# Kernel tuning notes

Hardware: AMD Instinct MI355X
Metric: run time of the kernel (lower is better)

Reference implementation:

```python
import jax, jax.numpy as jnp
import numpy as np

N, S, D, H, NF, E = 65536, 24, 64, 4, 256, 1048576
Hd = D // H
EPS = 1e-5


def _pe_table(nf, d):
    pe = np.zeros((nf, d), np.float32)
    pos = np.arange(nf, dtype=np.float32)[:, None]
    div = np.exp(np.arange(0, d, 2, dtype=np.float32) * -(np.log(10000.0) / d))
    pe[:, 0::2] = np.sin(pos * div)
    pe[:, 1::2] = np.cos(pos * div)
    return jnp.asarray(pe)


def setup_inputs() -> dict:
    key = jax.random.key(0)
    ks = iter(jax.random.split(key, 64))
    g = lambda shape: jax.random.normal(next(ks), shape, jnp.float32) * 0.02
    z = lambda shape: jnp.zeros(shape, jnp.float32)
    o = lambda shape: jnp.ones(shape, jnp.float32)
    inp = {
        'x': jax.random.normal(next(ks), (N, S), jnp.float32),
        'edge_index': jax.random.randint(next(ks), (2, E), 0, N, jnp.int32),
        'Wi': g((S, D)), 'bi': z((D,)), 'pe': _pe_table(NF, D),
        # per-head TransformerConv params (H separate convs, heads=1 each)
        'Wq': g((H, D, Hd)), 'Wk': g((H, D, Hd)), 'Wv': g((H, D, Hd)),
        'bq': z((H, Hd)), 'bk': z((H, Hd)), 'bv': z((H, Hd)),
        'Ws': g((H, D, Hd)), 'bs': z((H, Hd)),
        'Wo': g((D, D)), 'bo': z((D,)), 'gln_g': o((D,)), 'gln_b': z((D,)),
        # temporal MHA + FFN
        'Wqt': g((D, D)), 'Wkt': g((D, D)), 'Wvt': g((D, D)),
        'bqt': z((D,)), 'bkt': z((D,)), 'bvt': z((D,)),
        'Wot': g((D, D)), 'bot': z((D,)),
        'ln1_g': o((D,)), 'ln1_b': z((D,)),
        'W1': g((D, 2 * D)), 'b1': z((2 * D,)), 'W2': g((2 * D, D)), 'b2': z((D,)),
        'ln2_g': o((D,)), 'ln2_b': z((D,)),
        # aggregation + prediction head
        'Wa1': g((NF * D, D)), 'ba1': z((D,)), 'Wa2': g((D, D // 2)), 'ba2': z((D // 2,)),
        'Wh1': g((D // 2, D // 4)), 'bh1': z((D // 4,)), 'Wh2': g((D // 4, 1)), 'bh2': z((1,)),
    }
    return inp


def _ln(x, g, b):
    m = jnp.mean(x, axis=-1, keepdims=True)
    v = jnp.var(x, axis=-1, keepdims=True)
    return (x - m) * jax.lax.rsqrt(v + EPS) * g + b


def reference(x, edge_index, Wi, bi, pe, Wq, Wk, Wv, bq, bk, bv, Ws, bs, Wo, bo,
              gln_g, gln_b, Wqt, Wkt, Wvt, bqt, bkt, bvt, Wot, bot, ln1_g, ln1_b,
              W1, b1, W2, b2, ln2_g, ln2_b, Wa1, ba1, Wa2, ba2, Wh1, bh1, Wh2, bh2):
    n, nf, d = x.shape[0], pe.shape[0], pe.shape[1]
    bsz = n // nf
    scale = 1.0 / np.sqrt(Hd).astype(np.float32)

    # input projection + positional encoding (repeated per graph)
    h = x @ Wi + bi + jnp.tile(pe, (bsz, 1))  # [N, D]

    # ---- multi-head TransformerConv graph attention (gather-softmax-scatter) ----
    src, dst = edge_index[0], edge_index[1]
    q = jnp.einsum('nd,hdk->nhk', h, Wq) + bq  # [N,H,Hd]
    k = jnp.einsum('nd,hdk->nhk', h, Wk) + bk
    v = jnp.einsum('nd,hdk->nhk', h, Wv) + bv
    logits = jnp.sum(q[dst] * k[src], axis=-1) * scale  # [E,H]
    m = jax.ops.segment_max(logits, dst, num_segments=N)  # [N,H]
    ex = jnp.exp(logits - m[dst])
    denom = jax.ops.segment_sum(ex, dst, num_segments=N)  # [N,H]
    alpha = ex / denom[dst]
    agg = jax.ops.segment_sum(alpha[:, :, None] * v[src], dst, num_segments=N)  # [N,H,Hd]
    skip = jnp.einsum('nd,hdk->nhk', h, Ws) + bs  # root weight (lin_skip)
    out = (agg + skip).reshape(n, d) @ Wo + bo
    h = _ln(out + h, gln_g, gln_b)  # residual (in_dim == out_dim)

    # ---- temporal transformer over the NF node axis ----
    xt = h.reshape(bsz, nf, d)
    qt = (xt @ Wqt + bqt).reshape(bsz, nf, H, Hd)
    kt = (xt @ Wkt + bkt).reshape(bsz, nf, H, Hd)
    vt = (xt @ Wvt + bvt).reshape(bsz, nf, H, Hd)
    sc = jnp.einsum('bihd,bjhd->bhij', qt, kt) * scale
    a = jax.nn.softmax(sc, axis=-1)
    attn = jnp.einsum('bhij,bjhd->bihd', a, vt).reshape(bsz, nf, d)
    attn = attn @ Wot + bot
    xt = _ln(xt + attn, ln1_g, ln1_b)
    ff = jax.nn.relu(xt @ W1 + b1) @ W2 + b2
    xt = _ln(xt + ff, ln2_g, ln2_b)

    # ---- aggregation + prediction head ----
    xf = xt.reshape(bsz, nf * d)
    a1 = jax.nn.relu(xf @ Wa1 + ba1)
    a2 = jax.nn.relu(a1 @ Wa2 + ba2)
    h1 = jax.nn.relu(a2 @ Wh1 + bh1)
    out = jax.nn.sigmoid(h1 @ Wh2 + bh2)
    return out.squeeze(-1)  # [B]
```

## Files before the change

### kernel.cpp

```cpp
#include <hip/hip_runtime.h>
#include <hip/hip_fp16.h>
#include <math.h>

#define NN 65536
#define SIN 24
#define DD 64
#define HH 4
#define HDIM 16
#define NFRM 256
#define NE 1048576
#define BSZ 256
#define EPSLN 1e-5f
#define SCL 0.25f
#define AKS 32

typedef __attribute__((ext_vector_type(8))) short bf16x8;
typedef __attribute__((ext_vector_type(4))) float f32x4;

__device__ __forceinline__ unsigned short f2bf(float f) {
  unsigned u = __float_as_uint(f);
  return (unsigned short)((u + 0x7FFFu + ((u >> 16) & 1u)) >> 16);
}
__device__ __forceinline__ float bf2f(unsigned short b) {
  return __uint_as_float(((unsigned)b) << 16);
}
__device__ __forceinline__ float bflo(unsigned u) {
  return __uint_as_float(u << 16);
}
__device__ __forceinline__ float bfhi(unsigned u) {
  return __uint_as_float(u & 0xFFFF0000u);
}
__device__ __forceinline__ unsigned f2e5(float f) {
  unsigned short h = __half_as_ushort(__float2half(f));
  unsigned r = (unsigned)h + 0x7Fu + ((h >> 8) & 1u);
  return (r >> 8) & 0xFFu;
}
__device__ __forceinline__ float h2fb(unsigned short b) {
  return __half2float(__ushort_as_half(b));
}
#define KLO(u) h2fb((unsigned short)((u) & 0xFF00u))
#define KHI(u) h2fb((unsigned short)(((u) >> 16) & 0xFF00u))
#define VLO(u) h2fb((unsigned short)(((u) << 8) & 0xFF00u))
#define VHI(u) h2fb((unsigned short)(((u) >> 8) & 0xFF00u))

__device__ __forceinline__ void stage_bf(const unsigned short* __restrict__ src,
                                         unsigned short* dst, int n8, int DK, int ST, int tid) {
  int dk8 = DK >> 3;
  for (int idx = tid; idx < n8; idx += 256) {
    int row = idx / dk8, c = (idx % dk8) * 8;
    *(uint4*)(dst + row * ST + c) = *(const uint4*)(src + (size_t)row * DK + c);
  }
}

__global__ void k_wprep(const float* __restrict__ Wo, const float* __restrict__ Wot,
                        const float* __restrict__ Wqt, const float* __restrict__ Wkt,
                        const float* __restrict__ Wvt, const float* __restrict__ W1,
                        const float* __restrict__ W2, const float* __restrict__ Wq,
                        const float* __restrict__ Wk, const float* __restrict__ Wv,
                        const float* __restrict__ Wsk, unsigned short* __restrict__ wt) {
  int i = blockIdx.x * 256 + threadIdx.x;
  if (i >= 53248) return;
  float v;
  if (i < 4096)       { int t = i;         int j = t >> 6, d = t & 63; v = Wo[d * 64 + j]; }
  else if (i < 8192)  { int t = i - 4096;  int j = t >> 6, d = t & 63; v = Wot[d * 64 + j]; }
  else if (i < 12288) { int t = i - 8192;  int j = t >> 6, d = t & 63; v = Wqt[d * 64 + j]; }
  else if (i < 16384) { int t = i - 12288; int j = t >> 6, d = t & 63; v = Wkt[d * 64 + j]; }
  else if (i < 20480) { int t = i - 16384; int j = t >> 6, d = t & 63; v = Wvt[d * 64 + j]; }
  else if (i < 28672) { int t = i - 20480; int j = t >> 6, d = t & 63; v = W1[d * 128 + j]; }
  else if (i < 36864) { int t = i - 28672; int j = t >> 7, d = t & 127; v = W2[d * 64 + j]; }
  else if (i < 40960) { int t = i - 36864; int j = t >> 6, d = t & 63; v = Wq[(j >> 4) * 1024 + d * 16 + (j & 15)]; }
  else if (i < 45056) { int t = i - 40960; int j = t >> 6, d = t & 63; v = Wk[(j >> 4) * 1024 + d * 16 + (j & 15)]; }
  else if (i < 49152) { int t = i - 45056; int j = t >> 6, d = t & 63; v = Wv[(j >> 4) * 1024 + d * 16 + (j & 15)]; }
  else                { int t = i - 49152; int j = t >> 6, d = t & 63; v = Wsk[(j >> 4) * 1024 + d * 16 + (j & 15)]; }
  wt[i] = f2bf(v);
}

__global__ void k_wprep2(const float* __restrict__ Wa1, unsigned short* __restrict__ wa1t) {
  __shared__ float tile[64][65];
  int kb = blockIdx.x;
  int t = threadIdx.x;
  int c = t & 63, r0 = t >> 6;
  int k0 = kb * 64;
#pragma unroll
  for (int i = 0; i < 16; ++i) {
    int r = r0 + i * 4;
    tile[r][c] = Wa1[(size_t)(k0 + r) * 64 + c];
  }
  __syncthreads();
#pragma unroll
  for (int i = 0; i < 16; ++i) {
    int o = r0 + i * 4;
    wa1t[(size_t)o * 16384 + k0 + c] = f2bf(tile[c][o]);
  }
}

__global__ void __launch_bounds__(256)
k_qkvs_m(const float* __restrict__ x, const float* __restrict__ Wi,
         const float* __restrict__ bi, const float* __restrict__ pe,
         const unsigned short* __restrict__ wt,
         const float* __restrict__ bq, const float* __restrict__ bk,
         const float* __restrict__ bv, const float* __restrict__ bs,
         float* __restrict__ f_h, unsigned short* __restrict__ us_q,
         unsigned short* __restrict__ kv8, unsigned short* __restrict__ us_sk) {
  __shared__ unsigned short Xs[64 * 72];
  __shared__ unsigned short Ws4[4 * 64 * 72];
  float* Xs32 = (float*)Ws4;
  int tid = threadIdx.x;
  int n0 = blockIdx.x * 64;
  for (int idx = tid; idx < 64 * SIN; idx += 256) {
    int row = idx / SIN, c = idx % SIN;
    Xs32[row * 25 + c] = x[(size_t)(n0 + row) * SIN + c];
  }
  __syncthreads();
  int j = tid & 63, r0 = tid >> 6;
  float hacc[16];
  {
    float bb = bi[j];
#pragma unroll
    for (int i = 0; i < 16; ++i) {
      int row = r0 + 4 * i;
      hacc[i] = bb + pe[((n0 + row) & (NFRM - 1)) * DD + j];
    }
    for (int s = 0; s < SIN; ++s) {
      float w = Wi[s * DD + j];
#pragma unroll
      for (int i = 0; i < 16; ++i)
        hacc[i] += Xs32[(r0 + 4 * i) * 25 + s] * w;
    }
  }
  __syncthreads();
#pragma unroll
  for (int i = 0; i < 16; ++i) {
    int row = r0 + 4 * i;
    f_h[(size_t)(n0 + row) * DD + j] = hacc[i];
    Xs[row * 72 + j] = f2bf(hacc[i]);
  }
  stage_bf(wt + 36864, Ws4, 64 * 8, 64, 72, tid);
  stage_bf(wt + 40960, Ws4 + 4608, 64 * 8, 64, 72, tid);
  stage_bf(wt + 45056, Ws4 + 9216, 64 * 8, 64, 72, tid);
  stage_bf(wt + 49152, Ws4 + 13824, 64 * 8, 64, 72, tid);
  __syncthreads();
  int lane = tid & 63, w = tid >> 6;
  int c = lane & 15, g = lane >> 4;
  f32x4 aq[4], ak[4], av[4], as_[4];
#pragma unroll
  for (int jj = 0; jj < 4; ++jj) {
#pragma unroll
    for (int r = 0; r < 4; ++r) { aq[jj][r] = 0.f; ak[jj][r] = 0.f; av[jj][r] = 0.f; as_[jj][r] = 0.f; }
  }
  const unsigned short* xrow = Xs + (w * 16 + c) * 72 + g * 8;
#pragma unroll
  for (int kk = 0; kk < 2; ++kk) {
    bf16x8 af = *(const bf16x8*)(xrow + kk * 32);
#pragma unroll
    for (int jj = 0; jj < 4; ++jj) {
      int boff = (jj * 16 + c) * 72 + kk * 32 + g * 8;
      aq[jj] = __builtin_amdgcn_mfma_f32_16x16x32_bf16(af, *(const bf16x8*)(Ws4 + boff), aq[jj], 0, 0, 0);
      ak[jj] = __builtin_amdgcn_mfma_f32_16x16x32_bf16(af, *(const bf16x8*)(Ws4 + 4608 + boff), ak[jj], 0, 0, 0);
      av[jj] = __builtin_amdgcn_mfma_f32_16x16x32_bf16(af, *(const bf16x8*)(Ws4 + 9216 + boff), av[jj], 0, 0, 0);
      as_[jj] = __builtin_amdgcn_mfma_f32_16x16x32_bf16(af, *(const bf16x8*)(Ws4 + 13824 + boff), as_[jj], 0, 0, 0);
    }
  }
  int rowb = n0 + w * 16 + 4 * g;
#pragma unroll
  for (int jj = 0; jj < 4; ++jj) {
    int col = jj * 16 + c;
    float bqj = bq[col], bkj = bk[col], bvj = bv[col], bsj = bs[col];
#pragma unroll
    for (int r = 0; r < 4; ++r) {
      size_t o = (size_t)(rowb + r) * 64 + col;
      us_q[o] = f2bf(aq[jj][r] + bqj);
      kv8[o] = (unsigned short)((f2e5(ak[jj][r] + bkj) << 8) | f2e5(av[jj][r] + bvj));
      us_sk[o] = f2bf(as_[jj][r] + bsj);
    }
  }
}

__global__ void k_hist(const int* __restrict__ ei, int* __restrict__ hist) {
  __shared__ int h[256];
  int t = threadIdx.x;
  h[t] = 0;
  __syncthreads();
  int base = blockIdx.x * 4096;
#pragma unroll
  for (int r = 0; r < 16; ++r)
    atomicAdd(&h[ei[NE + base + r * 256 + t] >> 8], 1);
  __syncthreads();
  hist[t * 256 + blockIdx.x] = h[t];
}

__global__ void k_hscan(int* __restrict__ hist, int* __restrict__ btot) {
  __shared__ int s[256];
  int t = threadIdx.x, bkt = blockIdx.x;
  int v = hist[bkt * 256 + t];
  s[t] = v; __syncthreads();
  for (int off = 1; off < 256; off <<= 1) {
    int x = (t >= off) ? s[t - off] : 0;
    __syncthreads();
    s[t] += x;
    __syncthreads();
  }
  hist[bkt * 256 + t] = s[t] - v;
  if (t == 255) btot[bkt] = s[255];
}

__global__ void k_bscan(const int* __restrict__ btot, int* __restrict__ bbase) {
  __shared__ int s[256];
  int t = threadIdx.x;
  int v = btot[t];
  s[t] = v; __syncthreads();
  for (int off = 1; off < 256; off <<= 1) {
    int x = (t >= off) ? s[t - off] : 0;
    __syncthreads();
    s[t] += x;
    __syncthreads();
  }
  bbase[t] = s[t] - v;
}

__global__ void k_passB(const int* __restrict__ ei, const int* __restrict__ hist,
                        const int* __restrict__ bbase, int* __restrict__ pairs) {
  __shared__ int cur[256];
  int t = threadIdx.x;
  cur[t] = bbase[t] + hist[t * 256 + blockIdx.x];
  __syncthreads();
  int base = blockIdx.x * 4096;
#pragma unroll
  for (int r = 0; r < 16; ++r) {
    int e = base + r * 256 + t;
    int src = ei[e], dst = ei[NE + e];
    int pos = atomicAdd(&cur[dst >> 8], 1);
    pairs[pos] = ((dst & 255) << 16) | src;
  }
}

__global__ void k_passC(const int* __restrict__ pairs, const int* __restrict__ bbase,
                        const int* __restrict__ btot, int* __restrict__ rowptr,
                        int* __restrict__ srcs) {
  __shared__ int cnt[256];
  __shared__ int s[256];
  int t = threadIdx.x, bkt = blockIdx.x;
  cnt[t] = 0;
  __syncthreads();
  int base = bbase[bkt], n = btot[bkt];
  for (int i = t; i < n; i += 256) atomicAdd(&cnt[pairs[base + i] >> 16], 1);
  __syncthreads();
  int v = cnt[t];
  s[t] = v; __syncthreads();
  for (int off = 1; off < 256; off <<= 1) {
    int x = (t >= off) ? s[t - off] : 0;
    __syncthreads();
    s[t] += x;
    __syncthreads();
  }
  int rp = base + s[t] - v;
  rowptr[bkt * 256 + t] = rp;
  if (bkt == 0 && t == 0) rowptr[NN] = NE;
  __syncthreads();
  cnt[t] = rp;
  __syncthreads();
  for (int i = t; i < n; i += 256) {
    int p = pairs[base + i];
    int pos = atomicAdd(&cnt[p >> 16], 1);
    srcs[pos] = p & 0xFFFF;
  }
}

__global__ void __launch_bounds__(256)
k_gattn(const unsigned short* __restrict__ us_q, const unsigned short* __restrict__ kv8,
        const int* __restrict__ rowptr, const int* __restrict__ srcs,
        const unsigned short* __restrict__ us_sk, unsigned short* __restrict__ tmpb) {
  __shared__ float red[8][32][17];
  int tid = threadIdx.x;
  int lane = tid & 63;
  int slot = (tid >> 5) & 7;
  int e = (lane >> 2) & 7, h = lane & 3;
  int dst = (blockIdx.x << 3) + slot;
  float qv[16];
  {
    const uint4* qp = (const uint4*)(us_q + (size_t)dst * 64 + h * 16);
    uint4 q0 = qp[0], q1 = qp[1];
    qv[0] = bflo(q0.x); qv[1] = bfhi(q0.x); qv[2] = bflo(q0.y); qv[3] = bfhi(q0.y);
    qv[4] = bflo(q0.z); qv[5] = bfhi(q0.z); qv[6] = bflo(q0.w); qv[7] = bfhi(q0.w);
    qv[8] = bflo(q1.x); qv[9] = bfhi(q1.x); qv[10] = bflo(q1.y); qv[11] = bfhi(q1.y);
    qv[12] = bflo(q1.z); qv[13] = bfhi(q1.z); qv[14] = bflo(q1.w); qv[15] = bfhi(q1.w);
  }
  int beg = rowptr[dst], end = rowptr[dst + 1];
  float l = 0.f;
  float acc[16];
#pragma unroll
  for (int i = 0; i < 16; ++i) acc[i] = 0.f;

  int idx = beg + e;
  int src = (idx < end) ? srcs[idx] : 0;
  const uint4* kp = (const uint4*)(kv8 + (size_t)src * 64 + h * 16);
  uint4 A = kp[0], Bv = kp[1];
  for (;;) {
    int nidx = idx + 8;
    bool any_next = __any(nidx < end);
    uint4 nA, nB;
    if (any_next) {
      int nsrc = (nidx < end) ? srcs[nidx] : 0;
      const uint4* np = (const uint4*)(kv8 + (size_t)nsrc * 64 + h * 16);
      nA = np[0]; nB = np[1];
    }
    bool valid = idx < end;
    float s;
    s  = KLO(A.x) * qv[0]   + KHI(A.x) * qv[1]   + KLO(A.y) * qv[2]   + KHI(A.y) * qv[3];
    s += KLO(A.z) * qv[4]   + KHI(A.z) * qv[5]   + KLO(A.w) * qv[6]   + KHI(A.w) * qv[7];
    s += KLO(Bv.x) * qv[8]  + KHI(Bv.x) * qv[9]  + KLO(Bv.y) * qv[10] + KHI(Bv.y) * qv[11];
    s += KLO(Bv.z) * qv[12] + KHI(Bv.z) * qv[13] + KLO(Bv.w) * qv[14] + KHI(Bv.w) * qv[15];
    float pex = valid ? __expf(s * SCL) : 0.f;
    l += pex;
    acc[0]  += pex * VLO(A.x);  acc[1]  += pex * VHI(A.x);
    acc[2]  += pex * VLO(A.y);  acc[3]  += pex * VHI(A.y);
    acc[4]  += pex * VLO(A.z);  acc[5]  += pex * VHI(A.z);
    acc[6]  += pex * VLO(A.w);  acc[7]  += pex * VHI(A.w);
    acc[8]  += pex * VLO(Bv.x); acc[9]  += pex * VHI(Bv.x);
    acc[10] += pex * VLO(Bv.y); acc[11] += pex * VHI(Bv.y);
    acc[12] += pex * VLO(Bv.z); acc[13] += pex * VHI(Bv.z);
    acc[14] += pex * VLO(Bv.w); acc[15] += pex * VHI(Bv.w);
    if (!any_next) break;
    A = nA; Bv = nB;
    idx = nidx;
  }
  l += __shfl_xor(l, 4); l += __shfl_xor(l, 8); l += __shfl_xor(l, 16);
  float* rw = &red[slot][lane & 31][0];
#pragma unroll
  for (int i = 0; i < 16; ++i) rw[i] = acc[i];
  int r32 = lane & 31;
  int h0 = r32 >> 4, i0 = r32 & 15;
  float l0 = __shfl(l, (lane & 32) + h0);
  float l1 = __shfl(l, (lane & 32) + h0 + 2);
  float s0 = 0.f, s1 = 0.f;
#pragma unroll
  for (int ep = 0; ep < 8; ++ep) {
    s0 += red[slot][ep * 4 + h0][i0];
    s1 += red[slot][ep * 4 + h0 + 2][i0];
  }
  bool nonempty = end > beg;
  float a0 = nonempty ? s0 / l0 : 0.f;
  float a1 = nonempty ? s1 / l1 : 0.f;
  size_t o0 = (size_t)dst * 64 + r32;
  tmpb[o0] = f2bf(a0 + bf2f(us_sk[o0]));
  tmpb[o0 + 32] = f2bf(a1 + bf2f(us_sk[o0 + 32]));
}

__global__ void __launch_bounds__(256)
k_mlqkvt(const unsigned short* __restrict__ in1, const unsigned short* __restrict__ wt,
         const float* __restrict__ bias, const float* __restrict__ gam,
         const float* __restrict__ bet, float* __restrict__ io,
         const float* __restrict__ bqt, const float* __restrict__ bkt,
         const float* __restrict__ bvt,
         unsigned short* __restrict__ qt, unsigned short* __restrict__ kt,
         unsigned short* __restrict__ vt) {
  __shared__ unsigned short A[64 * 72];
  __shared__ unsigned short B[3 * 64 * 72];
  int tid = threadIdx.x;
  int n0 = blockIdx.x * 64;
  stage_bf(in1 + (size_t)n0 * 64, A, 64 * 8, 64, 72, tid);
  stage_bf(wt + 0, B, 64 * 8, 64, 72, tid);
  __syncthreads();
  int lane = tid & 63, w = tid >> 6;
  int c = lane & 15, g = lane >> 4;
  f32x4 acc[4];
#pragma unroll
  for (int j = 0; j < 4; ++j) { acc[j][0] = 0.f; acc[j][1] = 0.f; acc[j][2] = 0.f; acc[j][3] = 0.f; }
  const unsigned short* xrow = A + (w * 16 + c) * 72 + g * 8;
#pragma unroll
  for (int kk = 0; kk < 2; ++kk) {
    bf16x8 af = *(const bf16x8*)(xrow + kk * 32);
#pragma unroll
    for (int j = 0; j < 4; ++j)
      acc[j] = __builtin_amdgcn_mfma_f32_16x16x32_bf16(af,
                 *(const bf16x8*)(B + (j * 16 + c) * 72 + kk * 32 + g * 8), acc[j], 0, 0, 0);
  }
  int rowb = n0 + w * 16 + 4 * g;
  float o[4][4];
#pragma unroll
  for (int j = 0; j < 4; ++j) {
    int col = j * 16 + c;
    float bb = bias[col];
#pragma unroll
    for (int r = 0; r < 4; ++r)
      o[j][r] = acc[j][r] + bb + io[(size_t)(rowb + r) * 64 + col];
  }
#pragma unroll
  for (int r = 0; r < 4; ++r) {
    float s = (o[0][r] + o[1][r]) + (o[2][r] + o[3][r]);
    float s2 = (o[0][r] * o[0][r] + o[1][r] * o[1][r]) + (o[2][r] * o[2][r] + o[3][r] * o[3][r]);
#pragma unroll
    for (int off = 1; off <= 8; off <<= 1) {
      s += __shfl_xor(s, off);
      s2 += __shfl_xor(s2, off);
    }
    float mean = s * (1.0f / 64.0f);
    float var = s2 * (1.0f / 64.0f) - mean * mean;
    float rs = rsqrtf(var + EPSLN);
#pragma unroll
    for (int j = 0; j < 4; ++j)
      o[j][r] = (o[j][r] - mean) * rs * gam[j * 16 + c] + bet[j * 16 + c];
  }
  __syncthreads();
#pragma unroll
  for (int j = 0; j < 4; ++j) {
    int col = j * 16 + c;
#pragma unroll
    for (int r = 0; r < 4; ++r) {
      io[(size_t)(rowb + r) * 64 + col] = o[j][r];
      A[(w * 16 + 4 * g + r) * 72 + col] = f2bf(o[j][r]);
    }
  }
  stage_bf(wt + 8192, B, 64 * 8, 64, 72, tid);
  stage_bf(wt + 12288, B + 4608, 64 * 8, 64, 72, tid);
  stage_bf(wt + 16384, B + 9216, 64 * 8, 64, 72, tid);
  __syncthreads();
  f32x4 aq[4], ak[4], av[4];
#pragma unroll
  for (int j = 0; j < 4; ++j) {
#pragma unroll
    for (int r = 0; r < 4; ++r) { aq[j][r] = 0.f; ak[j][r] = 0.f; av[j][r] = 0.f; }
  }
#pragma unroll
  for (int kk = 0; kk < 2; ++kk) {
    bf16x8 af = *(const bf16x8*)(xrow + kk * 32);
#pragma unroll
    for (int j = 0; j < 4; ++j) {
      int boff = (j * 16 + c) * 72 + kk * 32 + g * 8;
      aq[j] = __builtin_amdgcn_mfma_f32_16x16x32_bf16(af, *(const bf16x8*)(B + boff), aq[j], 0, 0, 0);
      ak[j] = __builtin_amdgcn_mfma_f32_16x16x32_bf16(af, *(const bf16x8*)(B + 4608 + boff), ak[j], 0, 0, 0);
      av[j] = __builtin_amdgcn_mfma_f32_16x16x32_bf16(af, *(const bf16x8*)(B + 9216 + boff), av[j], 0, 0, 0);
    }
  }
#pragma unroll
  for (int j = 0; j < 4; ++j) {
    int col = j * 16 + c;
    float bqj = bqt[col], bkj = bkt[col], bvj = bvt[col];
#pragma unroll
    for (int r = 0; r < 4; ++r) {
      size_t oo = (size_t)(rowb + r) * 64 + col;
      qt[oo] = f2bf(aq[j][r] + bqj);
      kt[oo] = f2bf(ak[j][r] + bkj);
      vt[oo] = f2bf(av[j][r] + bvj);
    }
  }
}

#define VST 20
#define PST 40
__global__ void __launch_bounds__(256)
k_tattn(const unsigned short* __restrict__ qtb, const unsigned short* __restrict__ ktb,
        const unsigned short* __restrict__ vtb, unsigned short* __restrict__ attnb) {
  int b = blockIdx.x >> 2, hh = blockIdx.x & 3;
  __shared__ unsigned short Qs[NFRM][16];
  __shared__ unsigned short Ks[NFRM][16];
  __shared__ unsigned short Vs[NFRM][VST];
  __shared__ unsigned short Ps[4][16][PST];
  int t = threadIdx.x;
  int wv = t >> 6, lane = t & 63;
  int g = lane >> 4, c = lane & 15;
  {
    size_t src = ((size_t)b * NFRM + t) * DD + hh * 16;
    const uint4* qsrc = (const uint4*)(qtb + src);
    const uint4* ksrc = (const uint4*)(ktb + src);
    const uint2* vsrc = (const uint2*)(vtb + src);
    ((uint4*)Qs[t])[0] = qsrc[0]; ((uint4*)Qs[t])[1] = qsrc[1];
    ((uint4*)Ks[t])[0] = ksrc[0]; ((uint4*)Ks[t])[1] = ksrc[1];
    uint2* vdst = (uint2*)Vs[t];
    vdst[0] = vsrc[0]; vdst[1] = vsrc[1]; vdst[2] = vsrc[2]; vdst[3] = vsrc[3];
  }
  __syncthreads();
  const bf16x8 zf = {0, 0, 0, 0, 0, 0, 0, 0};
  unsigned short (*P)[PST] = Ps[wv];
  for (int qt0 = wv; qt0 < 16; qt0 += 4) {
    bf16x8 qf = zf;
    if (g < 2) qf = *(const bf16x8*)&Qs[qt0 * 16 + c][g * 8];
    f32x4 O = {0.f, 0.f, 0.f, 0.f};
    float lacc[4] = {0.f, 0.f, 0.f, 0.f};
    for (int jp = 0; jp < 8; ++jp) {
#pragma unroll
      for (int half = 0; half < 2; ++half) {
        int jt = jp * 2 + half;
        bf16x8 kf = zf;
        if (g < 2) kf = *(const bf16x8*)&Ks[jt * 16 + c][g * 8];
        f32x4 S = __builtin_amdgcn_mfma_f32_16x16x32_bf16(qf, kf,
                    (f32x4){0.f, 0.f, 0.f, 0.f}, 0, 0, 0);
#pragma unroll
        for (int r = 0; r < 4; ++r) {
          float p = __expf(S[r] * SCL);
          lacc[r] += p;
          P[4 * g + r][half * 16 + c] = f2bf(p);
        }
      }
      bf16x8 pf = *(const bf16x8*)&P[c][g * 8];
      bf16x8 vf;
#pragma unroll
      for (int i = 0; i < 8; ++i) vf[i] = (short)Vs[jp * 32 + g * 8 + i][c];
      O = __builtin_amdgcn_mfma_f32_16x16x32_bf16(pf, vf, O, 0, 0, 0);
    }
#pragma unroll
    for (int r = 0; r < 4; ++r) {
      float s = lacc[r];
      s += __shfl_xor(s, 1); s += __shfl_xor(s, 2);
      s += __shfl_xor(s, 4); s += __shfl_xor(s, 8);
      lacc[r] = 1.0f / s;
    }
    size_t obase = ((size_t)b * NFRM + qt0 * 16) * DD + hh * 16;
#pragma unroll
    for (int r = 0; r < 4; ++r)
      attnb[obase + (size_t)(4 * g + r) * DD + c] = f2bf(O[r] * lacc[r]);
  }
}

__global__ void __launch_bounds__(256)
k_blk2(const unsigned short* __restrict__ attn, const unsigned short* __restrict__ wt,
       const float* __restrict__ res, const float* __restrict__ bot,
       const float* __restrict__ l1g, const float* __restrict__ l1b,
       const float* __restrict__ b1, const float* __restrict__ b2,
       const float* __restrict__ l2g, const float* __restrict__ l2b,
       unsigned short* __restrict__ xtb) {
  __shared__ unsigned short XLs[64 * 72];
  __shared__ unsigned short BufW[128 * 72];
  __shared__ unsigned short BufX[64 * 136];
  int tid = threadIdx.x;
  int n0 = blockIdx.x * 64;
  int lane = tid & 63, w = tid >> 6;
  int c = lane & 15, g = lane >> 4;
  int rowb = n0 + w * 16 + 4 * g;
  stage_bf(attn + (size_t)n0 * 64, BufX, 64 * 8, 64, 72, tid);
  stage_bf(wt + 4096, BufW, 64 * 8, 64, 72, tid);
  __syncthreads();
  f32x4 acc[4];
#pragma unroll
  for (int j = 0; j < 4; ++j) { acc[j][0] = 0.f; acc[j][1] = 0.f; acc[j][2] = 0.f; acc[j][3] = 0.f; }
  const unsigned short* xrow = BufX + (w * 16 + c) * 72 + g * 8;
#pragma unroll
  for (int kk = 0; kk < 2; ++kk) {
    bf16x8 af = *(const bf16x8*)(xrow + kk * 32);
#pragma unroll
    for (int j = 0; j < 4; ++j)
      acc[j] = __builtin_amdgcn_mfma_f32_16x16x32_bf16(af,
                 *(const bf16x8*)(BufW + (j * 16 + c) * 72 + kk * 32 + g * 8), acc[j], 0, 0, 0);
  }
  float x[4][4];
#pragma unroll
  for (int j = 0; j < 4; ++j) {
    int col = j * 16 + c;
    float bb = bot[col];
#pragma unroll
    for (int r = 0; r < 4; ++r)
      x[j][r] = acc[j][r] + bb + res[(size_t)(rowb + r) * 64 + col];
  }
#pragma unroll
  for (int r = 0; r < 4; ++r) {
    float s = (x[0][r] + x[1][r]) + (x[2][r] + x[3][r]);
    float s2 = (x[0][r] * x[0][r] + x[1][r] * x[1][r]) + (x[2][r] * x[2][r] + x[3][r] * x[3][r]);
#pragma unroll
    for (int off = 1; off <= 8; off <<= 1) {
      s += __shfl_xor(s, off);
      s2 += __shfl_xor(s2, off);
    }
    float mean = s * (1.0f / 64.0f);
    float var = s2 * (1.0f / 64.0f) - mean * mean;
    float rs = rsqrtf(var + EPSLN);
#pragma unroll
    for (int j = 0; j < 4; ++j)
      x[j][r] = (x[j][r] - mean) * rs * l1g[j * 16 + c] + l1b[j * 16 + c];
  }
  __syncthreads();
#pragma unroll
  for (int j = 0; j < 4; ++j)
#pragma unroll
    for (int r = 0; r < 4; ++r)
      XLs[(w * 16 + 4 * g + r) * 72 + j * 16 + c] = f2bf(x[j][r]);
  stage_bf(wt + 20480, BufW, 128 * 8, 64, 72, tid);
  __syncthreads();
  f32x4 ua[8];
#pragma unroll
  for (int j = 0; j < 8; ++j) { ua[j][0] = 0.f; ua[j][1] = 0.f; ua[j][2] = 0.f; ua[j][3] = 0.f; }
  const unsigned short* xrow2 = XLs + (w * 16 + c) * 72 + g * 8;
#pragma unroll
  for (int kk = 0; kk < 2; ++kk) {
    bf16x8 af = *(const bf16x8*)(xrow2 + kk * 32);
#pragma unroll
    for (int j = 0; j < 8; ++j)
      ua[j] = __builtin_amdgcn_mfma_f32_16x16x32_bf16(af,
                *(const bf16x8*)(BufW + (j * 16 + c) * 72 + kk * 32 + g * 8), ua[j], 0, 0, 0);
  }
#pragma unroll
  for (int j = 0; j < 8; ++j) {
    int col = j * 16 + c;
    float bb = b1[col];
#pragma unroll
    for (int r = 0; r < 4; ++r)
      BufX[(w * 16 + 4 * g + r) * 136 + col] = f2bf(fmaxf(ua[j][r] + bb, 0.f));
  }
  __syncthreads();
  stage_bf(wt + 28672, BufW, 64 * 16, 128, 136, tid);
  __syncthreads();
  f32x4 ya[4];
#pragma unroll
  for (int j = 0; j < 4; ++j) { ya[j][0] = 0.f; ya[j][1] = 0.f; ya[j][2] = 0.f; ya[j][3] = 0.f; }
  const unsigned short* urow = BufX + (w * 16 + c) * 136 + g * 8;
#pragma unroll
  for (int kk = 0; kk < 4; ++kk) {
    bf16x8 af = *(const bf16x8*)(urow + kk * 32);
#pragma unroll
    for (int j = 0; j < 4; ++j)
      ya[j] = __builtin_amdgcn_mfma_f32_16x16x32_bf16(af,
                *(const bf16x8*)(BufW + (j * 16 + c) * 136 + kk * 32 + g * 8), ya[j], 0, 0, 0);
  }
  float o2[4][4];
#pragma unroll
  for (int j = 0; j < 4; ++j) {
    int col = j * 16 + c;
    float bb = b2[col];
#pragma unroll
    for (int r = 0; r < 4; ++r)
      o2[j][r] = ya[j][r] + bb + x[j][r];
  }
#pragma unroll
  for (int r = 0; r < 4; ++r) {
    float s = (o2[0][r] + o2[1][r]) + (o2[2][r] + o2[3][r]);
    float s2 = (o2[0][r] * o2[0][r] + o2[1][r] * o2[1][r]) + (o2[2][r] * o2[2][r] + o2[3][r] * o2[3][r]);
#pragma unroll
    for (int off = 1; off <= 8; off <<= 1) {
      s += __shfl_xor(s, off);
      s2 += __shfl_xor(s2, off);
    }
    float mean = s * (1.0f / 64.0f);
    float var = s2 * (1.0f / 64.0f) - mean * mean;
    float rs = rsqrtf(var + EPSLN);
#pragma unroll
    for (int j = 0; j < 4; ++j)
      xtb[(size_t)(rowb + r) * 64 + j * 16 + c] =
          f2bf((o2[j][r] - mean) * rs * l2g[j * 16 + c] + l2b[j * 16 + c]);
  }
}

__global__ void __launch_bounds__(256)
k_agg1a_m(const unsigned short* __restrict__ xtb, const unsigned short* __restrict__ wa1t,
          float* __restrict__ part) {
  int ks = blockIdx.x >> 2, mt = blockIdx.x & 3;
  int t = threadIdx.x, lane = t & 63, w = t >> 6;
  int c = lane & 15, g = lane >> 4;
  int m0 = mt * 64;
  int k0 = ks * 512;
  f32x4 acc[4];
#pragma unroll
  for (int j = 0; j < 4; ++j) { acc[j][0] = 0.f; acc[j][1] = 0.f; acc[j][2] = 0.f; acc[j][3] = 0.f; }
  const unsigned short* arow = xtb + (size_t)(m0 + w * 16 + c) * 16384 + k0 + g * 8;
  const unsigned short* brow = wa1t + (size_t)c * 16384 + k0 + g * 8;
#pragma unroll 4
  for (int kk = 0; kk < 16; ++kk) {
    bf16x8 af = *(const bf16x8*)(arow + kk * 32);
#pragma unroll
    for (int j = 0; j < 4; ++j)
      acc[j] = __builtin_amdgcn_mfma_f32_16x16x32_bf16(af,
                 *(const bf16x8*)(brow + (size_t)j * 16 * 16384 + kk * 32), acc[j], 0, 0, 0);
  }
  int rowb = m0 + w * 16 + 4 * g;
#pragma unroll
  for (int j = 0; j < 4; ++j)
#pragma unroll
    for (int r = 0; r < 4; ++r)
      part[(size_t)ks * (BSZ * DD) + (size_t)(rowb + r) * 64 + j * 16 + c] = acc[j][r];
}

__global__ void k_head(const float* __restrict__ part, const float* __restrict__ ba1,
                       const float* __restrict__ Wa2, const float* __restrict__ ba2,
                       const float* __restrict__ Wh1, const float* __restrict__ bh1,
                       const float* __restrict__ Wh2, const float* __restrict__ bh2,
                       float* __restrict__ out) {
  int b = blockIdx.x, t = threadIdx.x;
  __shared__ float s1[64], s2[32], s3[16];
  float a0 = ba1[t];
#pragma unroll 8
  for (int ks = 0; ks < AKS; ++ks) a0 += part[(size_t)ks * (BSZ * DD) + b * 64 + t];
  s1[t] = fmaxf(a0, 0.f);
  __syncthreads();
  if (t < 32) {
    float a = ba2[t];
#pragma unroll 8
    for (int j = 0; j < 64; ++j) a += s1[j] * Wa2[j * 32 + t];
    s2[t] = fmaxf(a, 0.f);
  }
  __syncthreads();
  if (t < 16) {
    float a = bh1[t];
#pragma unroll
    for (int j = 0; j < 32; ++j) a += s2[j] * Wh1[j * 16 + t];
    s3[t] = fmaxf(a, 0.f);
  }
  __syncthreads();
  if (t == 0) {
    float a = bh2[0];
#pragma unroll
    for (int j = 0; j < 16; ++j) a += s3[j] * Wh2[j];
    out[b] = 1.0f / (1.0f + expf(-a));
  }
}

extern "C" void kernel_launch(void* const* d_in, const int* in_sizes, int n_in,
                              void* d_out, int out_size, void* d_ws, size_t ws_size,
                              hipStream_t stream) {
  const float* x   = (const float*)d_in[0];
  const int*   ei  = (const int*)d_in[1];
  const float* Wi  = (const float*)d_in[2];
  const float* bi  = (const float*)d_in[3];
  const float* pe  = (const float*)d_in[4];
  const float* Wq  = (const float*)d_in[5];
  const float* Wk  = (const float*)d_in[6];
  const float* Wv  = (const float*)d_in[7];
  const float* bq  = (const float*)d_in[8];
  const float* bk  = (const float*)d_in[9];
  const float* bv  = (const float*)d_in[10];
  const float* Ws  = (const float*)d_in[11];
  const float* bs  = (const float*)d_in[12];
  const float* Wo  = (const float*)d_in[13];
  const float* bo  = (const float*)d_in[14];
  const float* gg  = (const float*)d_in[15];
  const float* gb  = (const float*)d_in[16];
  const float* Wqt = (const float*)d_in[17];
  const float* Wkt = (const float*)d_in[18];
  const float* Wvt = (const float*)d_in[19];
  const float* bqt = (const float*)d_in[20];
  const float* bkt = (const float*)d_in[21];
  const float* bvt = (const float*)d_in[22];
  const float* Wot = (const float*)d_in[23];
  const float* bot = (const float*)d_in[24];
  const float* l1g = (const float*)d_in[25];
  const float* l1b = (const float*)d_in[26];
  const float* W1  = (const float*)d_in[27];
  const float* b1  = (const float*)d_in[28];
  const float* W2  = (const float*)d_in[29];
  const float* b2  = (const float*)d_in[30];
  const float* l2g = (const float*)d_in[31];
  const float* l2b = (const float*)d_in[32];
  const float* Wa1 = (const float*)d_in[33];
  const float* ba1 = (const float*)d_in[34];
  const float* Wa2 = (const float*)d_in[35];
  const float* ba2 = (const float*)d_in[36];
  const float* Wh1 = (const float*)d_in[37];
  const float* bh1 = (const float*)d_in[38];
  const float* Wh2 = (const float*)d_in[39];
  const float* bh2 = (const float*)d_in[40];
  float* out = (float*)d_out;

  const size_t ND = (size_t)NN * DD;

  float* wsf = (float*)d_ws;
  float* f_h = wsf;
  unsigned short* us_q  = (unsigned short*)(f_h + ND);
  unsigned short* kv8   = us_q + ND;
  unsigned short* us_sk = kv8 + ND;
  unsigned short* tmpb  = us_sk + ND;
  unsigned short* us_qt = tmpb + ND;
  unsigned short* us_kt = us_qt + ND;
  unsigned short* us_vt = us_kt + ND;
  unsigned short* attnb = us_vt + ND;
  unsigned short* xtb   = attnb + ND;
  float* f_part = (float*)(xtb + ND);
  int* i_srcs   = (int*)(f_part + (size_t)AKS * BSZ * DD);
  int* i_rowptr = i_srcs + NE;
  int* i_hist   = i_rowptr + NN + 1;
  int* i_btot   = i_hist + 65536;
  int* i_bbase  = i_btot + 256;
  int* i_pairs  = i_bbase + 256;
  unsigned short* wt = (unsigned short*)(i_pairs + NE);
  unsigned short* wa1t = wt + 53248;

  dim3 B(256);
  k_wprep<<<dim3(208), B, 0, stream>>>(Wo, Wot, Wqt, Wkt, Wvt, W1, W2, Wq, Wk, Wv, Ws, wt);
  k_wprep2<<<dim3(256), B, 0, stream>>>(Wa1, wa1t);
  k_qkvs_m<<<dim3(NN / 64), B, 0, stream>>>(x, Wi, bi, pe, wt, bq, bk, bv, bs,
                                            f_h, us_q, kv8, us_sk);
  k_hist <<<dim3(256), B, 0, stream>>>(ei, i_hist);
  k_hscan<<<dim3(256), B, 0, stream>>>(i_hist, i_btot);
  k_bscan<<<dim3(1),   B, 0, stream>>>(i_btot, i_bbase);
  k_passB<<<dim3(256), B, 0, stream>>>(ei, i_hist, i_bbase, i_pairs);
  k_passC<<<dim3(256), B, 0, stream>>>(i_pairs, i_bbase, i_btot, i_rowptr, i_srcs);
  k_gattn<<<dim3(NN / 8), B, 0, stream>>>(us_q, kv8, i_rowptr, i_srcs, us_sk, tmpb);
  k_mlqkvt<<<dim3(NN / 64), B, 0, stream>>>(tmpb, wt, bo, gg, gb, f_h,
                                            bqt, bkt, bvt, us_qt, us_kt, us_vt);
  k_tattn<<<dim3(BSZ * HH), B, 0, stream>>>(us_qt, us_kt, us_vt, attnb);
  k_blk2<<<dim3(NN / 64), B, 0, stream>>>(attnb, wt, f_h, bot, l1g, l1b, b1, b2,
                                          l2g, l2b, xtb);
  k_agg1a_m<<<dim3(AKS * 4), B, 0, stream>>>(xtb, wa1t, f_part);
  k_head<<<dim3(BSZ), dim3(64), 0, stream>>>(f_part, ba1, Wa2, ba2, Wh1, bh1, Wh2, bh2, out);
}
```

Measured before the change: 183.2 us.

## Store residual h in bf16, MFMA input projection, split histogram, register-cache pairs

The fp32 residual buffer f_h becomes a bf16 buffer, which halves the residual traffic in three kernels (qkvs, mlqkvt, blk2). The input projection x@Wi now runs on MFMA with bf16 weights that are prepacked in k_wprep. k_hist splits its shared histogram into two copies to cut atomic contention, and k_passC keeps up to 18 pairs per thread in registers so the second pass does not reload them. The residual now carries bf16 rounding error, which lowers accuracy.

```diff
diff --git a/kernel.cpp b/kernel.cpp
--- a/kernel.cpp
+++ b/kernel.cpp
@@ -13,6 +13,7 @@
 #define EPSLN 1e-5f
 #define SCL 0.25f
 #define AKS 32
+#define WTN 55296
 
 typedef __attribute__((ext_vector_type(8))) short bf16x8;
 typedef __attribute__((ext_vector_type(4))) float f32x4;
@@ -57,9 +58,10 @@
                         const float* __restrict__ Wvt, const float* __restrict__ W1,
                         const float* __restrict__ W2, const float* __restrict__ Wq,
                         const float* __restrict__ Wk, const float* __restrict__ Wv,
-                        const float* __restrict__ Wsk, unsigned short* __restrict__ wt) {
+                        const float* __restrict__ Wsk, const float* __restrict__ Wi,
+                        unsigned short* __restrict__ wt) {
   int i = blockIdx.x * 256 + threadIdx.x;
-  if (i >= 53248) return;
+  if (i >= WTN) return;
   float v;
   if (i < 4096)       { int t = i;         int j = t >> 6, d = t & 63; v = Wo[d * 64 + j]; }
   else if (i < 8192)  { int t = i - 4096;  int j = t >> 6, d = t & 63; v = Wot[d * 64 + j]; }
@@ -71,7 +73,8 @@
   else if (i < 40960) { int t = i - 36864; int j = t >> 6, d = t & 63; v = Wq[(j >> 4) * 1024 + d * 16 + (j & 15)]; }
   else if (i < 45056) { int t = i - 40960; int j = t >> 6, d = t & 63; v = Wk[(j >> 4) * 1024 + d * 16 + (j & 15)]; }
   else if (i < 49152) { int t = i - 45056; int j = t >> 6, d = t & 63; v = Wv[(j >> 4) * 1024 + d * 16 + (j & 15)]; }
-  else                { int t = i - 49152; int j = t >> 6, d = t & 63; v = Wsk[(j >> 4) * 1024 + d * 16 + (j & 15)]; }
+  else if (i < 53248) { int t = i - 49152; int j = t >> 6, d = t & 63; v = Wsk[(j >> 4) * 1024 + d * 16 + (j & 15)]; }
+  else                { int t = i - 53248; int j = t >> 5, k = t & 31; v = (k < SIN) ? Wi[k * 64 + j] : 0.f; }
   wt[i] = f2bf(v);
 }
 
@@ -95,53 +98,55 @@
 }
 
 __global__ void __launch_bounds__(256)
-k_qkvs_m(const float* __restrict__ x, const float* __restrict__ Wi,
+k_qkvs_m(const float* __restrict__ x, const unsigned short* __restrict__ wt,
          const float* __restrict__ bi, const float* __restrict__ pe,
-         const unsigned short* __restrict__ wt,
          const float* __restrict__ bq, const float* __restrict__ bk,
          const float* __restrict__ bv, const float* __restrict__ bs,
-         float* __restrict__ f_h, unsigned short* __restrict__ us_q,
+         unsigned short* __restrict__ us_h, unsigned short* __restrict__ us_q,
          unsigned short* __restrict__ kv8, unsigned short* __restrict__ us_sk) {
   __shared__ unsigned short Xs[64 * 72];
   __shared__ unsigned short Ws4[4 * 64 * 72];
-  float* Xs32 = (float*)Ws4;
+  unsigned short* Xi  = Ws4;
+  unsigned short* WiS = Ws4 + 64 * 40;
   int tid = threadIdx.x;
   int n0 = blockIdx.x * 64;
-  for (int idx = tid; idx < 64 * SIN; idx += 256) {
-    int row = idx / SIN, c = idx % SIN;
-    Xs32[row * 25 + c] = x[(size_t)(n0 + row) * SIN + c];
-  }
-  __syncthreads();
-  int j = tid & 63, r0 = tid >> 6;
-  float hacc[16];
+  for (int idx = tid; idx < 2048; idx += 256) {
+    int row = idx >> 5, k = idx & 31;
+    Xi[row * 40 + k] = (k < SIN) ? f2bf(x[(size_t)(n0 + row) * SIN + k]) : 0;
+    WiS[row * 40 + k] = wt[53248 + row * 32 + k];
+  }
+  __syncthreads();
+  int lane = tid & 63, w = tid >> 6;
+  int c = lane & 15, g = lane >> 4;
+  int rowb = n0 + w * 16 + 4 * g;
+  f32x4 hb[4];
   {
-    float bb = bi[j];
-#pragma unroll
-    for (int i = 0; i < 16; ++i) {
-      int row = r0 + 4 * i;
-      hacc[i] = bb + pe[((n0 + row) & (NFRM - 1)) * DD + j];
-    }
-    for (int s = 0; s < SIN; ++s) {
-      float w = Wi[s * DD + j];
-#pragma unroll
-      for (int i = 0; i < 16; ++i)
-        hacc[i] += Xs32[(r0 + 4 * i) * 25 + s] * w;
-    }
-  }
-  __syncthreads();
-#pragma unroll
-  for (int i = 0; i < 16; ++i) {
-    int row = r0 + 4 * i;
-    f_h[(size_t)(n0 + row) * DD + j] = hacc[i];
-    Xs[row * 72 + j] = f2bf(hacc[i]);
-  }
+    bf16x8 xf = *(const bf16x8*)(Xi + (w * 16 + c) * 40 + g * 8);
+#pragma unroll
+    for (int jj = 0; jj < 4; ++jj)
+      hb[jj] = __builtin_amdgcn_mfma_f32_16x16x32_bf16(xf,
+                 *(const bf16x8*)(WiS + (jj * 16 + c) * 40 + g * 8),
+                 (f32x4){0.f, 0.f, 0.f, 0.f}, 0, 0, 0);
+  }
+#pragma unroll
+  for (int jj = 0; jj < 4; ++jj) {
+    int col = jj * 16 + c;
+    float bb = bi[col];
+#pragma unroll
+    for (int r = 0; r < 4; ++r) {
+      int row = w * 16 + 4 * g + r;
+      float hv = hb[jj][r] + bb + pe[((n0 + row) & (NFRM - 1)) * DD + col];
+      unsigned short hbf = f2bf(hv);
+      us_h[(size_t)(n0 + row) * DD + col] = hbf;
+      Xs[row * 72 + col] = hbf;
+    }
+  }
+  __syncthreads();
   stage_bf(wt + 36864, Ws4, 64 * 8, 64, 72, tid);
   stage_bf(wt + 40960, Ws4 + 4608, 64 * 8, 64, 72, tid);
   stage_bf(wt + 45056, Ws4 + 9216, 64 * 8, 64, 72, tid);
   stage_bf(wt + 49152, Ws4 + 13824, 64 * 8, 64, 72, tid);
   __syncthreads();
-  int lane = tid & 63, w = tid >> 6;
-  int c = lane & 15, g = lane >> 4;
   f32x4 aq[4], ak[4], av[4], as_[4];
 #pragma unroll
   for (int jj = 0; jj < 4; ++jj) {
@@ -161,7 +166,6 @@
       as_[jj] = __builtin_amdgcn_mfma_f32_16x16x32_bf16(af, *(const bf16x8*)(Ws4 + 13824 + boff), as_[jj], 0, 0, 0);
     }
   }
-  int rowb = n0 + w * 16 + 4 * g;
 #pragma unroll
   for (int jj = 0; jj < 4; ++jj) {
     int col = jj * 16 + c;
@@ -177,16 +181,17 @@
 }
 
 __global__ void k_hist(const int* __restrict__ ei, int* __restrict__ hist) {
-  __shared__ int h[256];
+  __shared__ int h2[2][256];
   int t = threadIdx.x;
-  h[t] = 0;
-  __syncthreads();
+  h2[0][t] = 0; h2[1][t] = 0;
+  __syncthreads();
+  int sub = (t >> 6) & 1;
   int base = blockIdx.x * 4096;
 #pragma unroll
   for (int r = 0; r < 16; ++r)
-    atomicAdd(&h[ei[NE + base + r * 256 + t] >> 8], 1);
-  __syncthreads();
-  hist[t * 256 + blockIdx.x] = h[t];
+    atomicAdd(&h2[sub][ei[NE + base + r * 256 + t] >> 8], 1);
+  __syncthreads();
+  hist[t * 256 + blockIdx.x] = h2[0][t] + h2[1][t];
 }
 
 __global__ void k_hscan(int* __restrict__ hist, int* __restrict__ btot) {
@@ -243,7 +248,17 @@
   cnt[t] = 0;
   __syncthreads();
   int base = bbase[bkt], n = btot[bkt];
-  for (int i = t; i < n; i += 256) atomicAdd(&cnt[pairs[base + i] >> 16], 1);
+  int pr[18];
+#pragma unroll
+  for (int j = 0; j < 18; ++j) {
+    int i = t + j * 256;
+    if (i >= n) break;
+    int p = pairs[base + i];
+    pr[j] = p;
+    atomicAdd(&cnt[p >> 16], 1);
+  }
+  for (int i = t + 18 * 256; i < n; i += 256)
+    atomicAdd(&cnt[pairs[base + i] >> 16], 1);
   __syncthreads();
   int v = cnt[t];
   s[t] = v; __syncthreads();
@@ -259,7 +274,15 @@
   __syncthreads();
   cnt[t] = rp;
   __syncthreads();
-  for (int i = t; i < n; i += 256) {
+#pragma unroll
+  for (int j = 0; j < 18; ++j) {
+    int i = t + j * 256;
+    if (i >= n) break;
+    int p = pr[j];
+    int pos = atomicAdd(&cnt[p >> 16], 1);
+    srcs[pos] = p & 0xFFFF;
+  }
+  for (int i = t + 18 * 256; i < n; i += 256) {
     int p = pairs[base + i];
     int pos = atomicAdd(&cnt[p >> 16], 1);
     srcs[pos] = p & 0xFFFF;
@@ -349,7 +372,7 @@
 __global__ void __launch_bounds__(256)
 k_mlqkvt(const unsigned short* __restrict__ in1, const unsigned short* __restrict__ wt,
          const float* __restrict__ bias, const float* __restrict__ gam,
-         const float* __restrict__ bet, float* __restrict__ io,
+         const float* __restrict__ bet, unsigned short* __restrict__ us_h,
          const float* __restrict__ bqt, const float* __restrict__ bkt,
          const float* __restrict__ bvt,
          unsigned short* __restrict__ qt, unsigned short* __restrict__ kt,
@@ -383,7 +406,7 @@
     float bb = bias[col];
 #pragma unroll
     for (int r = 0; r < 4; ++r)
-      o[j][r] = acc[j][r] + bb + io[(size_t)(rowb + r) * 64 + col];
+      o[j][r] = acc[j][r] + bb + bf2f(us_h[(size_t)(rowb + r) * 64 + col]);
   }
 #pragma unroll
   for (int r = 0; r < 4; ++r) {
@@ -407,8 +430,9 @@
     int col = j * 16 + c;
 #pragma unroll
     for (int r = 0; r < 4; ++r) {
-      io[(size_t)(rowb + r) * 64 + col] = o[j][r];
-      A[(w * 16 + 4 * g + r) * 72 + col] = f2bf(o[j][r]);
+      unsigned short ob = f2bf(o[j][r]);
+      us_h[(size_t)(rowb + r) * 64 + col] = ob;
+      A[(w * 16 + 4 * g + r) * 72 + col] = ob;
     }
   }
   stage_bf(wt + 8192, B, 64 * 8, 64, 72, tid);
@@ -514,7 +538,7 @@
 
 __global__ void __launch_bounds__(256)
 k_blk2(const unsigned short* __restrict__ attn, const unsigned short* __restrict__ wt,
-       const float* __restrict__ res, const float* __restrict__ bot,
+       const unsigned short* __restrict__ res, const float* __restrict__ bot,
        const float* __restrict__ l1g, const float* __restrict__ l1b,
        const float* __restrict__ b1, const float* __restrict__ b2,
        const float* __restrict__ l2g, const float* __restrict__ l2b,
@@ -549,7 +573,7 @@
     float bb = bot[col];
 #pragma unroll
     for (int r = 0; r < 4; ++r)
-      x[j][r] = acc[j][r] + bb + res[(size_t)(rowb + r) * 64 + col];
+      x[j][r] = acc[j][r] + bb + bf2f(res[(size_t)(rowb + r) * 64 + col]);
   }
 #pragma unroll
   for (int r = 0; r < 4; ++r) {
@@ -749,9 +773,8 @@
 
   const size_t ND = (size_t)NN * DD;
 
-  float* wsf = (float*)d_ws;
-  float* f_h = wsf;
-  unsigned short* us_q  = (unsigned short*)(f_h + ND);
+  unsigned short* us_h  = (unsigned short*)d_ws;
+  unsigned short* us_q  = us_h + ND;
   unsigned short* kv8   = us_q + ND;
   unsigned short* us_sk = kv8 + ND;
   unsigned short* tmpb  = us_sk + ND;
@@ -763,28 +786,29 @@
   float* f_part = (float*)(xtb + ND);
   int* i_srcs   = (int*)(f_part + (size_t)AKS * BSZ * DD);
   int* i_rowptr = i_srcs + NE;
-  int* i_hist   = i_rowptr + NN + 1;
+  int* i_hist   = i_rowptr + NN + 4;
   int* i_btot   = i_hist + 65536;
   int* i_bbase  = i_btot + 256;
   int* i_pairs  = i_bbase + 256;
   unsigned short* wt = (unsigned short*)(i_pairs + NE);
-  unsigned short* wa1t = wt + 53248;
+  unsigned short* wa1t = wt + WTN;
 
   dim3 B(256);
-  k_wprep<<<dim3(208), B, 0, stream>>>(Wo, Wot, Wqt, Wkt, Wvt, W1, W2, Wq, Wk, Wv, Ws, wt);
+  k_wprep<<<dim3((WTN + 255) / 256), B, 0, stream>>>(Wo, Wot, Wqt, Wkt, Wvt, W1, W2,
+                                                     Wq, Wk, Wv, Ws, Wi, wt);
   k_wprep2<<<dim3(256), B, 0, stream>>>(Wa1, wa1t);
-  k_qkvs_m<<<dim3(NN / 64), B, 0, stream>>>(x, Wi, bi, pe, wt, bq, bk, bv, bs,
-                                            f_h, us_q, kv8, us_sk);
+  k_qkvs_m<<<dim3(NN / 64), B, 0, stream>>>(x, wt, bi, pe, bq, bk, bv, bs,
+                                            us_h, us_q, kv8, us_sk);
   k_hist <<<dim3(256), B, 0, stream>>>(ei, i_hist);
   k_hscan<<<dim3(256), B, 0, stream>>>(i_hist, i_btot);
   k_bscan<<<dim3(1),   B, 0, stream>>>(i_btot, i_bbase);
   k_passB<<<dim3(256), B, 0, stream>>>(ei, i_hist, i_bbase, i_pairs);
   k_passC<<<dim3(256), B, 0, stream>>>(i_pairs, i_bbase, i_btot, i_rowptr, i_srcs);
   k_gattn<<<dim3(NN / 8), B, 0, stream>>>(us_q, kv8, i_rowptr, i_srcs, us_sk, tmpb);
-  k_mlqkvt<<<dim3(NN / 64), B, 0, stream>>>(tmpb, wt, bo, gg, gb, f_h,
+  k_mlqkvt<<<dim3(NN / 64), B, 0, stream>>>(tmpb, wt, bo, gg, gb, us_h,
                                             bqt, bkt, bvt, us_qt, us_kt, us_vt);
   k_tattn<<<dim3(BSZ * HH), B, 0, stream>>>(us_qt, us_kt, us_vt, attnb);
-  k_blk2<<<dim3(NN / 64), B, 0, stream>>>(attnb, wt, f_h, bot, l1g, l1b, b1, b2,
+  k_blk2<<<dim3(NN / 64), B, 0, stream>>>(attnb, wt, us_h, bot, l1g, l1b, b1, b2,
                                           l2g, l2b, xtb);
   k_agg1a_m<<<dim3(AKS * 4), B, 0, stream>>>(xtb, wa1t, f_part);
   k_head<<<dim3(BSZ), dim3(64), 0, stream>>>(f_part, ba1, Wa2, ba2, Wh1, bh1, Wh2, bh2, out);
```

New measurement: 178.7 us. -2.5%, faster.
